# Optimization experiments

Measured on AMD Instinct MI355X. Metric: run time of the kernel, lower is better.

Reference implementation:

```python
import jax, jax.numpy as jnp
import numpy as np

SIGMA = 25.0
N, E, F, D = 10000, 160000, 256, 3


def setup_inputs() -> dict:
    key = jax.random.key(0)
    ks = jax.random.split(key, 24)
    s = 0.02
    inp = {
        "x": jax.random.normal(ks[0], (N, D), jnp.float32),
        "edge_index": jax.random.randint(ks[1], (2, E), 0, N, jnp.int64),
        "t": jax.random.uniform(ks[2], (N, 1), jnp.float32, 1e-3, 1.0),
        "emb_pcs": jax.random.normal(ks[3], (N, F), jnp.float32),
        # x_encoder
        "enc_W": jax.random.normal(ks[4], (D, F), jnp.float32) * s,
        "enc_b": jnp.zeros((F,), jnp.float32),
        # GaussianFourierProjection (scale=30, fixed) + Linear
        "fourier_W": jax.random.normal(ks[5], (F // 2,), jnp.float32) * 30.0,
        "te_W": jax.random.normal(ks[6], (F, F), jnp.float32) * s,
        "te_b": jnp.zeros((F,), jnp.float32),
        # mlp1 / mlp2: Linear(6F,F) -> ReLU -> Linear(F,F)
        "m1_W1": jax.random.normal(ks[7], (6 * F, F), jnp.float32) * s,
        "m1_b1": jnp.zeros((F,), jnp.float32),
        "m1_W2": jax.random.normal(ks[8], (F, F), jnp.float32) * s,
        "m1_b2": jnp.zeros((F,), jnp.float32),
        "m2_W1": jax.random.normal(ks[9], (6 * F, F), jnp.float32) * s,
        "m2_b1": jnp.zeros((F,), jnp.float32),
        "m2_W2": jax.random.normal(ks[10], (F, F), jnp.float32) * s,
        "m2_b2": jnp.zeros((F,), jnp.float32),
        # mlp3: Linear(6F,F) -> ReLU -> Linear(F,D)
        "m3_W1": jax.random.normal(ks[11], (6 * F, F), jnp.float32) * s,
        "m3_b1": jnp.zeros((F,), jnp.float32),
        "m3_W2": jax.random.normal(ks[12], (F, D), jnp.float32) * s,
        "m3_b2": jnp.zeros((D,), jnp.float32),
    }
    return inp


def _edge_conv(h, src, dst, W1, b1, W2, b2, n):
    # PyG EdgeConv: out_i = max_{j->i} MLP([x_i, x_j - x_i])
    hi = h[dst]                                             # [E, 3F]
    e = jnp.concatenate([hi, h[src] - hi], axis=-1)         # [E, 6F]
    e = jax.nn.relu(e @ W1 + b1) @ W2 + b2                  # [E, out]
    out = jax.ops.segment_max(e, dst, num_segments=n)
    return jnp.where(jnp.isfinite(out), out, 0.0)           # empty segments -> 0


def reference(x, edge_index, t, emb_pcs,
              enc_W, enc_b, fourier_W, te_W, te_b,
              m1_W1, m1_b1, m1_W2, m1_b2,
              m2_W1, m2_b1, m2_W2, m2_b2,
              m3_W1, m3_b1, m3_W2, m3_b2):
    src, dst = edge_index[0], edge_index[1]
    n = x.shape[0]
    # time embedding: Fourier projection -> Linear -> swish
    tv = t[:, 0]
    proj = tv[:, None] * fourier_W[None, :] * (2.0 * np.pi)  # [N, F/2]
    temb = jnp.concatenate([jnp.sin(proj), jnp.cos(proj)], axis=-1) @ te_W + te_b
    temb = temb * jax.nn.sigmoid(temb)                       # [N, F]
    h = x @ enc_W + enc_b                                    # [N, F]
    h = jnp.concatenate([h, temb, emb_pcs], axis=-1)         # [N, 3F]
    h = jax.nn.relu(_edge_conv(h, src, dst, m1_W1, m1_b1, m1_W2, m1_b2, n))
    h = jnp.concatenate([h, temb, emb_pcs], axis=-1)
    h = jax.nn.relu(_edge_conv(h, src, dst, m2_W1, m2_b1, m2_W2, m2_b2, n))
    h = jnp.concatenate([h, temb, emb_pcs], axis=-1)
    h = _edge_conv(h, src, dst, m3_W1, m3_b1, m3_W2, m3_b2, n)  # [N, D]
    # marginal_prob_std(t) = sqrt((sigma^(2t) - 1) / (2 ln sigma))
    std = jnp.sqrt((jnp.power(SIGMA, 2.0 * t) - 1.0) / (2.0 * jnp.log(SIGMA)))
    return h / (std + 1e-7)
```

## Files before the change

### kernel.cpp

```cpp
#include <hip/hip_runtime.h>
#include <hip/hip_bf16.h>
#include <math.h>

#define HC 768
#define DPB 8

typedef __attribute__((ext_vector_type(8))) short bf16x8;
typedef __attribute__((ext_vector_type(4))) float f32x4;

__device__ __forceinline__ float bf2f(unsigned short h) {
    return __uint_as_float(((unsigned)h) << 16);
}
__device__ __forceinline__ unsigned short f2bf(float f) {
    unsigned u = __float_as_uint(f);
    return (unsigned short)((u + 0x7fffu + ((u >> 16) & 1u)) >> 16);
}
__device__ __forceinline__ unsigned pack_bf2(float a, float b) {
    __hip_bfloat162 h = __float22bfloat162_rn(make_float2(a, b));
    return *reinterpret_cast<unsigned*>(&h);
}

__device__ __forceinline__ unsigned enc_f(float f) {
    unsigned u = __float_as_uint(f);
    return (u & 0x80000000u) ? ~u : (u | 0x80000000u);
}
__device__ __forceinline__ float dec_f(unsigned e) {
    unsigned u = (e & 0x80000000u) ? (e & 0x7FFFFFFFu) : ~e;
    return __uint_as_float(u);
}
#define ENC_NEG_INF 0x007FFFFFu

__global__ void pre_and_prep_kernel(const float* __restrict__ x,
                                    const float* __restrict__ t,
                                    const float* __restrict__ emb,
                                    const float* __restrict__ enc_W,
                                    const float* __restrict__ enc_b,
                                    const float* __restrict__ fw,
                                    const float* __restrict__ te_W,
                                    const float* __restrict__ te_b,
                                    unsigned short* __restrict__ hcat,
                                    float* __restrict__ invstd,
                                    const float* __restrict__ W1a,
                                    const float* __restrict__ W1b,
                                    const float* __restrict__ W1c,
                                    const float* __restrict__ W2a,
                                    const float* __restrict__ W2b,
                                    const float* __restrict__ W2c,
                                    unsigned short* __restrict__ WcatT,
                                    unsigned short* __restrict__ W2T,
                                    unsigned short* __restrict__ W2T3,
                                    int N, int nPre) {
    __shared__ float smem[64 * 65];
    const int tid = threadIdx.x;

    if ((int)blockIdx.x < nPre) {
        float (*ti)[256] = (float(*)[256])smem;
        float* tv = smem + 8 * 256;
        const int n0 = blockIdx.x * 8;

        if (tid < 8) {
            int n = n0 + tid;
            float tt = (n < N) ? t[n] : 1.0f;
            tv[tid] = tt;
            const float ln_s = 3.2188758248682006f;
            float p = expf(2.0f * tt * ln_s);
            float sd = sqrtf((p - 1.0f) / (2.0f * ln_s));
            if (n < N) invstd[n] = 1.0f / (sd + 1e-7f);
        }
        __syncthreads();

        const float TWO_PI = 6.283185307179586f;
        for (int p = tid; p < 8 * 128; p += 256) {
            int n = p >> 7, j = p & 127;
            float pr = tv[n] * fw[j] * TWO_PI;
            ti[n][j]       = sinf(pr);
            ti[n][j + 128] = cosf(pr);
        }
        __syncthreads();

        const int j = tid;
        float acc[8];
#pragma unroll
        for (int n = 0; n < 8; ++n) acc[n] = 0.f;
        for (int k = 0; k < 256; ++k) {
            float w = te_W[k * 256 + j];
#pragma unroll
            for (int n = 0; n < 8; ++n) acc[n] += ti[n][k] * w;
        }
        float bj  = te_b[j];
        float ew0 = enc_W[0 * 256 + j], ew1 = enc_W[1 * 256 + j], ew2 = enc_W[2 * 256 + j];
        float ebj = enc_b[j];
        for (int n = 0; n < 8; ++n) {
            int node = n0 + n;
            if (node >= N) break;
            float v = acc[n] + bj;
            float temb = v / (1.0f + expf(-v));
            float h0 = x[node * 3 + 0] * ew0 + x[node * 3 + 1] * ew1 +
                       x[node * 3 + 2] * ew2 + ebj;
            hcat[(size_t)node * HC + j]       = f2bf(h0);
            hcat[(size_t)node * HC + 256 + j] = f2bf(temb);
            hcat[(size_t)node * HC + 512 + j] = f2bf(emb[node * 256 + j]);
        }
    } else {
        float (*buf)[65] = (float(*)[65])smem;
        const int bid = blockIdx.x - nPre;
        const int tx = tid & 63, ty = tid >> 6;

        if (bid < 288) {
            const int l = bid / 96, r = bid - l * 96;
            const float* W1 = (l == 0) ? W1a : (l == 1) ? W1b : W1c;
            unsigned short* WT = WcatT + (size_t)l * 512 * 768;
            const int k0 = (r % 12) * 64, n0 = (r / 12) * 64;
#pragma unroll
            for (int i = 0; i < 16; ++i) {
                int kl = ty + i * 4;
                int k = k0 + kl, n = n0 + tx;
                float v = (n < 256) ? (W1[(size_t)k * 256 + n] - W1[(size_t)(k + 768) * 256 + n])
                                    : W1[(size_t)(k + 768) * 256 + (n - 256)];
                buf[kl][tx] = v;
            }
            __syncthreads();
#pragma unroll
            for (int i = 0; i < 16; ++i) {
                int nl = ty + i * 4;
                WT[(size_t)(n0 + nl) * 768 + k0 + tx] = f2bf(buf[tx][nl]);
            }
        } else if (bid < 320) {
            const int m = bid - 288, l = m >> 4, r = m & 15;
            const float* W2 = (l == 0) ? W2a : W2b;
            unsigned short* WT = W2T + (size_t)l * 256 * 256;
            const int k0 = (r & 3) * 64, n0 = (r >> 2) * 64;
#pragma unroll
            for (int i = 0; i < 16; ++i) {
                int kl = ty + i * 4;
                buf[kl][tx] = W2[(size_t)(k0 + kl) * 256 + n0 + tx];
            }
            __syncthreads();
#pragma unroll
            for (int i = 0; i < 16; ++i) {
                int nl = ty + i * 4;
                WT[(size_t)(n0 + nl) * 256 + k0 + tx] = f2bf(buf[tx][nl]);
            }
        } else {
            int idx = (bid - 320) * 256 + tid;
            int n = idx >> 8, k = idx & 255;
            W2T3[idx] = (n < 3) ? f2bf(W2c[(size_t)k * 3 + n]) : (unsigned short)0;
        }
    }
}

__global__ __launch_bounds__(256)
void node_gemm_mfma_kernel(const unsigned short* __restrict__ A,
                           const unsigned short* __restrict__ BT,
                           const float* __restrict__ b1,
                           unsigned short* __restrict__ C,
                           int M) {
    const int row0 = blockIdx.x * 64, col0 = blockIdx.y * 128;
    const int tid = threadIdx.x;
    const int wv = tid >> 6, lane = tid & 63;
    const int q = lane >> 4, nl = lane & 15;
    const int rbase = row0 + (wv >> 1) * 32;
    const int cbase = col0 + (wv & 1) * 64;

    int r0c = min(rbase + nl, M - 1);
    int r1c = min(rbase + 16 + nl, M - 1);
    const unsigned short* pa0 = A + (size_t)r0c * HC + q * 8;
    const unsigned short* pa1 = A + (size_t)r1c * HC + q * 8;

    f32x4 acc[2][4];
#pragma unroll
    for (int s = 0; s < 2; ++s)
#pragma unroll
        for (int t = 0; t < 4; ++t) acc[s][t] = (f32x4){0.f, 0.f, 0.f, 0.f};

    for (int ks = 0; ks < 24; ++ks) {
        const int k0 = ks * 32;
        const bf16x8 av0 = *(const bf16x8*)(pa0 + k0);
        const bf16x8 av1 = *(const bf16x8*)(pa1 + k0);
#pragma unroll
        for (int t = 0; t < 4; ++t) {
            const bf16x8 bv = *(const bf16x8*)(BT + (size_t)(cbase + t * 16 + nl) * 768 + k0 + q * 8);
            acc[0][t] = __builtin_amdgcn_mfma_f32_16x16x32_bf16(av0, bv, acc[0][t], 0, 0, 0);
            acc[1][t] = __builtin_amdgcn_mfma_f32_16x16x32_bf16(av1, bv, acc[1][t], 0, 0, 0);
        }
    }

#pragma unroll
    for (int s = 0; s < 2; ++s) {
        const int rr = rbase + s * 16 + q * 4;
#pragma unroll
        for (int t = 0; t < 4; ++t) {
            int col = cbase + t * 16 + nl;
            float bb = (col < 256) ? b1[col] : 0.f;
#pragma unroll
            for (int i = 0; i < 4; ++i) {
                int r = rr + i;
                if (r < M) C[(size_t)r * 512 + col] = f2bf(acc[s][t][i] + bb);
            }
        }
    }
}

__global__ void init_kernel(unsigned* __restrict__ cnt, unsigned* __restrict__ seg3, int N) {
    int idx = blockIdx.x * 256 + threadIdx.x;
    if (idx < 2 * N) cnt[idx] = 0u;
    else if (idx < 5 * N) seg3[idx - 2 * N] = ENC_NEG_INF;
}
__global__ void hist_kernel(const int* __restrict__ dst, unsigned* __restrict__ cnt, int E) {
    int e = blockIdx.x * 256 + threadIdx.x;
    if (e < E) atomicAdd(&cnt[dst[e]], 1u);
}
__global__ void scan_kernel(const unsigned* __restrict__ cnt,
                            int* __restrict__ row_start, int N) {
    __shared__ unsigned buf[1024];
    __shared__ unsigned carry;
    const int tid = threadIdx.x;
    if (tid == 0) carry = 0u;
    __syncthreads();
    for (int base = 0; base < N; base += 1024) {
        int i = base + tid;
        unsigned v = (i < N) ? cnt[i] : 0u;
        buf[tid] = v;
        __syncthreads();
#pragma unroll
        for (int off = 1; off < 1024; off <<= 1) {
            unsigned add = (tid >= off) ? buf[tid - off] : 0u;
            __syncthreads();
            buf[tid] += add;
            __syncthreads();
        }
        if (i < N) row_start[i] = (int)(carry + buf[tid] - v);
        __syncthreads();
        if (tid == 0) carry += buf[1023];
        __syncthreads();
    }
    if (tid == 0) row_start[N] = (int)carry;
}
__global__ void scatter_kernel(const int* __restrict__ src, const int* __restrict__ dst,
                               const int* __restrict__ row_start,
                               unsigned* __restrict__ wcnt,
                               int* __restrict__ es, int* __restrict__ ed, int E) {
    int e = blockIdx.x * 256 + threadIdx.x;
    if (e >= E) return;
    int d = dst[e];
    int pos = row_start[d] + (int)atomicAdd(&wcnt[d], 1u);
    es[pos] = src[e];
    ed[pos] = d;
}

__global__ __launch_bounds__(256, 3)
void edge_seg_gemm_kernel(const unsigned short* __restrict__ RQb,
                          const int* __restrict__ es,
                          const int* __restrict__ ed,
                          const int* __restrict__ row_start,
                          const unsigned short* __restrict__ W2T,
                          const float* __restrict__ b2,
                          unsigned short* __restrict__ hcat,
                          int N, int E) {
    __shared__ unsigned short af[64][264];
    __shared__ unsigned short rdst[DPB][256];
    __shared__ unsigned lseg[DPB * 256];
    __shared__ int ss[64], sdl[64];
    const int d0 = blockIdx.x * DPB;
    const int tid = threadIdx.x;
    const int wv = tid >> 6, lane = tid & 63;
    const int q = lane >> 4, nl = lane & 15;

    for (int i = tid; i < DPB * 256; i += 256) lseg[i] = ENC_NEG_INF;

    {
        int rrow = tid >> 5;
        int kc = (tid & 31) * 8;
        int d = d0 + rrow;
        int dc = (d < N) ? d : (N - 1);
        *(bf16x8*)&rdst[rrow][kc] = *(const bf16x8*)(RQb + (size_t)dc * 512 + kc);
    }

    const int eBeg = row_start[d0];
    const int eEnd = row_start[min(d0 + DPB, N)];

    for (int c0 = eBeg; c0 < eEnd; c0 += 64) {
        __syncthreads();
        if (tid < 64) {
            int e = c0 + tid;
            ss[tid]  = (e < eEnd) ? es[e] : 0;
            sdl[tid] = (e < eEnd) ? (ed[e] - d0) : -1;
        }
        __syncthreads();

        {
            const int el = tid >> 2;
            const int kc = (tid & 3) * 64;
            int dl = sdl[el];
            int dla = (dl >= 0) ? dl : 0;
            int srow = ss[el];
            const unsigned short* ps = RQb + (size_t)srow * 512 + 256 + kc;
#pragma unroll
            for (int j = 0; j < 8; ++j) {
                bf16x8 dv = *(const bf16x8*)&rdst[dla][kc + j * 8];
                bf16x8 sv = *(const bf16x8*)(ps + j * 8);
                float f[8];
#pragma unroll
                for (int u = 0; u < 8; ++u)
                    f[u] = fmaxf(bf2f((unsigned short)dv[u]) + bf2f((unsigned short)sv[u]), 0.f);
                uint4 o;
                o.x = pack_bf2(f[0], f[1]);
                o.y = pack_bf2(f[2], f[3]);
                o.z = pack_bf2(f[4], f[5]);
                o.w = pack_bf2(f[6], f[7]);
                *(uint4*)&af[el][kc + j * 8] = o;
            }
        }
        __syncthreads();

#pragma unroll
        for (int sub = 0; sub < 4; ++sub) {
            f32x4 acc[4];
#pragma unroll
            for (int t = 0; t < 4; ++t) acc[t] = (f32x4){0.f, 0.f, 0.f, 0.f};
#pragma unroll
            for (int ks = 0; ks < 8; ++ks) {
                const bf16x8 av = *(const bf16x8*)&af[sub * 16 + nl][ks * 32 + q * 8];
#pragma unroll
                for (int t = 0; t < 4; ++t) {
                    const bf16x8 bv = *(const bf16x8*)(W2T +
                        (size_t)(wv * 64 + t * 16 + nl) * 256 + ks * 32 + q * 8);
                    acc[t] = __builtin_amdgcn_mfma_f32_16x16x32_bf16(av, bv, acc[t], 0, 0, 0);
                }
            }
            const int m0 = sub * 16 + q * 4;
            int dls[4];
#pragma unroll
            for (int i = 0; i < 4; ++i) dls[i] = sdl[m0 + i];
#pragma unroll
            for (int t = 0; t < 4; ++t) {
                const int col = wv * 64 + t * 16 + nl;
                float cur = -INFINITY;
                int cd = dls[0];
#pragma unroll
                for (int i = 0; i < 4; ++i) {
                    int dl = dls[i];
                    if (dl != cd) {
                        if (cd >= 0) atomicMax(&lseg[cd * 256 + col], enc_f(cur));
                        cur = -INFINITY; cd = dl;
                    }
                    cur = fmaxf(cur, acc[t][i]);
                }
                if (cd >= 0) atomicMax(&lseg[cd * 256 + col], enc_f(cur));
            }
        }
    }
    __syncthreads();

    for (int i = tid; i < DPB * 256; i += 256) {
        int dl = i >> 8, col = i & 255;
        int d = d0 + dl;
        if (d >= N) continue;
        float f = dec_f(lseg[i]);
        float v = isfinite(f) ? fmaxf(f + b2[col], 0.f) : 0.f;
        hcat[(size_t)d * HC + col] = f2bf(v);
    }
}

__global__ __launch_bounds__(256)
void edge3_mfma_kernel(const unsigned short* __restrict__ RQb,
                       const int* __restrict__ es,
                       const int* __restrict__ ed,
                       const unsigned short* __restrict__ W2T3,
                       const float* __restrict__ b2,
                       unsigned* __restrict__ seg3,
                       int E) {
    const int wave = blockIdx.x * 4 + (threadIdx.x >> 6);
    const int lane = threadIdx.x & 63;
    const int q = lane >> 4, nl = lane & 15;
    const int e0 = wave * 16;
    if (e0 >= E) return;

    bf16x8 bv[8];
#pragma unroll
    for (int ks = 0; ks < 8; ++ks)
        bv[ks] = *(const bf16x8*)(W2T3 + (size_t)nl * 256 + ks * 32 + q * 8);

    int eA = e0 + nl;
    int eAc = (eA < E) ? eA : (E - 1);
    const int dA = ed[eAc], sA = es[eAc];
    const unsigned short* pd = RQb + (size_t)dA * 512 + q * 8;
    const unsigned short* ps = RQb + (size_t)sA * 512 + 256 + q * 8;

    f32x4 acc = (f32x4){0.f, 0.f, 0.f, 0.f};
#pragma unroll
    for (int ks = 0; ks < 8; ++ks) {
        bf16x8 dv = *(const bf16x8*)(pd + ks * 32);
        bf16x8 sv = *(const bf16x8*)(ps + ks * 32);
        float f[8];
#pragma unroll
        for (int u = 0; u < 8; ++u)
            f[u] = fmaxf(bf2f((unsigned short)dv[u]) + bf2f((unsigned short)sv[u]), 0.f);
        uint4 o;
        o.x = pack_bf2(f[0], f[1]);
        o.y = pack_bf2(f[2], f[3]);
        o.z = pack_bf2(f[4], f[5]);
        o.w = pack_bf2(f[6], f[7]);
        bf16x8 av = *(bf16x8*)&o;
        acc = __builtin_amdgcn_mfma_f32_16x16x32_bf16(av, bv[ks], acc, 0, 0, 0);
    }

    if (nl < 3) {
        float bb = b2[nl];
        float cur = -INFINITY;
        int cd = -2;
#pragma unroll
        for (int i = 0; i < 4; ++i) {
            int e = e0 + q * 4 + i;
            int d = (e < E) ? ed[e] : -1;
            if (d != cd) {
                if (cd >= 0) atomicMax(&seg3[(size_t)cd * 3 + nl], enc_f(cur + bb));
                cur = -INFINITY; cd = d;
            }
            if (d >= 0) cur = fmaxf(cur, acc[i]);
        }
        if (cd >= 0) atomicMax(&seg3[(size_t)cd * 3 + nl], enc_f(cur + bb));
    }
}

__global__ void finalize3_kernel(const unsigned* __restrict__ seg3,
                                 const float* __restrict__ invstd,
                                 float* __restrict__ out, int N) {
    int idx = blockIdx.x * 256 + threadIdx.x;
    if (idx >= N * 3) return;
    int n = idx / 3;
    float f = dec_f(seg3[idx]);
    if (!isfinite(f)) f = 0.f;
    out[idx] = f * invstd[n];
}

extern "C" void kernel_launch(void* const* d_in, const int* in_sizes, int n_in,
                              void* d_out, int out_size, void* d_ws, size_t ws_size,
                              hipStream_t stream) {
    const float* x     = (const float*)d_in[0];
    const int*   ei    = (const int*)d_in[1];
    const float* t     = (const float*)d_in[2];
    const float* emb   = (const float*)d_in[3];
    const float* enc_W = (const float*)d_in[4];
    const float* enc_b = (const float*)d_in[5];
    const float* fw    = (const float*)d_in[6];
    const float* te_W  = (const float*)d_in[7];
    const float* te_b  = (const float*)d_in[8];
    const float* W1[3] = {(const float*)d_in[9],  (const float*)d_in[13], (const float*)d_in[17]};
    const float* b1[3] = {(const float*)d_in[10], (const float*)d_in[14], (const float*)d_in[18]};
    const float* W2[3] = {(const float*)d_in[11], (const float*)d_in[15], (const float*)d_in[19]};
    const float* b2[3] = {(const float*)d_in[12], (const float*)d_in[16], (const float*)d_in[20]};

    const int N = in_sizes[2];
    const int E = in_sizes[1] / 2;
    const int* src = ei;
    const int* dst = ei + E;

    char* ws = (char*)d_ws;
    unsigned short* hcat  = (unsigned short*)ws; ws += (size_t)N * HC * 2;
    unsigned short* RQb   = (unsigned short*)ws; ws += (size_t)N * 512 * 2;
    unsigned short* WcatT = (unsigned short*)ws; ws += (size_t)3 * 512 * 768 * 2;
    unsigned short* W2T   = (unsigned short*)ws; ws += (size_t)2 * 256 * 256 * 2;
    unsigned short* W2T3  = (unsigned short*)ws; ws += (size_t)16 * 256 * 2;
    unsigned* seg3        = (unsigned*)ws;       ws += (size_t)N * 3 * 4;
    float*    invstd      = (float*)ws;          ws += (size_t)N * 4;
    int*      es          = (int*)ws;            ws += (size_t)E * 4;
    int*      ed          = (int*)ws;            ws += (size_t)E * 4;
    unsigned* cnt         = (unsigned*)ws;       ws += (size_t)N * 4;
    unsigned* wcnt        = (unsigned*)ws;       ws += (size_t)N * 4;
    int*      row_start   = (int*)ws;            ws += (size_t)(N + 1) * 4;

    init_kernel<<<(5 * N + 255) / 256, 256, 0, stream>>>(cnt, seg3, N);
    hist_kernel<<<(E + 255) / 256, 256, 0, stream>>>(dst, cnt, E);
    scan_kernel<<<1, 1024, 0, stream>>>(cnt, row_start, N);
    scatter_kernel<<<(E + 255) / 256, 256, 0, stream>>>(src, dst, row_start, wcnt, es, ed, E);

    const int nPre = (N + 7) / 8;
    pre_and_prep_kernel<<<nPre + 336, 256, 0, stream>>>(
        x, t, emb, enc_W, enc_b, fw, te_W, te_b, hcat, invstd,
        W1[0], W1[1], W1[2], W2[0], W2[1], W2[2], WcatT, W2T, W2T3, N, nPre);

    for (int l = 0; l < 3; ++l) {
        dim3 gn((N + 63) / 64, 4);
        node_gemm_mfma_kernel<<<gn, 256, 0, stream>>>(
            hcat, WcatT + (size_t)l * 512 * 768, b1[l], RQb, N);
        if (l < 2) {
            edge_seg_gemm_kernel<<<(N + DPB - 1) / DPB, 256, 0, stream>>>(
                RQb, es, ed, row_start, W2T + (size_t)l * 256 * 256, b2[l], hcat, N, E);
        } else {
            int chunks = (E + 15) / 16;
            edge3_mfma_kernel<<<(chunks + 3) / 4, 256, 0, stream>>>(
                RQb, es, ed, W2T3, b2[l], seg3, E);
            finalize3_kernel<<<(N * 3 + 255) / 256, 256, 0, stream>>>(seg3, invstd, (float*)d_out, N);
        }
    }
}
```

Measured before the change: 503.0 us.

## Double-buffer edge tiles with register prefetch and use wave-shuffle scan

Restructures the edge segment GEMM to process edges in 32-row chunks with a double-buffered LDS A tile. The source-row gathers for the next chunk are prefetched into registers while the current chunk's MFMAs run, and one sync per chunk is removed. The shared src/dst index staging is dropped: destination indices are read directly from global memory in the epilogue. Separately, the scan kernel's log-step shared-memory scan with many barriers is replaced by a wave-level shuffle scan plus a small cross-wave scan.

```diff
diff --git a/kernel.cpp b/kernel.cpp
--- a/kernel.cpp
+++ b/kernel.cpp
@@ -212,26 +212,38 @@
 }
 __global__ void scan_kernel(const unsigned* __restrict__ cnt,
                             int* __restrict__ row_start, int N) {
-    __shared__ unsigned buf[1024];
+    __shared__ unsigned wexc[16];
+    __shared__ unsigned chunk_total;
     __shared__ unsigned carry;
-    const int tid = threadIdx.x;
+    const int tid = threadIdx.x, wv = tid >> 6, ln = tid & 63;
     if (tid == 0) carry = 0u;
     __syncthreads();
     for (int base = 0; base < N; base += 1024) {
         int i = base + tid;
         unsigned v = (i < N) ? cnt[i] : 0u;
-        buf[tid] = v;
-        __syncthreads();
-#pragma unroll
-        for (int off = 1; off < 1024; off <<= 1) {
-            unsigned add = (tid >= off) ? buf[tid - off] : 0u;
-            __syncthreads();
-            buf[tid] += add;
-            __syncthreads();
-        }
-        if (i < N) row_start[i] = (int)(carry + buf[tid] - v);
-        __syncthreads();
-        if (tid == 0) carry += buf[1023];
+        unsigned s = v;
+#pragma unroll
+        for (int off = 1; off < 64; off <<= 1) {
+            unsigned o = __shfl_up(s, off);
+            if (ln >= off) s += o;
+        }
+        if (ln == 63) wexc[wv] = s;
+        __syncthreads();
+        if (tid < 16) {
+            unsigned ws = wexc[tid];
+            unsigned tt = ws;
+#pragma unroll
+            for (int off = 1; off < 16; off <<= 1) {
+                unsigned o = __shfl_up(tt, off);
+                if (tid >= off) tt += o;
+            }
+            wexc[tid] = tt - ws;
+            if (tid == 15) chunk_total = tt;
+        }
+        __syncthreads();
+        if (i < N) row_start[i] = (int)(carry + wexc[wv] + s - v);
+        __syncthreads();
+        if (tid == 0) carry += chunk_total;
         __syncthreads();
     }
     if (tid == 0) row_start[N] = (int)carry;
@@ -257,10 +269,9 @@
                           const float* __restrict__ b2,
                           unsigned short* __restrict__ hcat,
                           int N, int E) {
-    __shared__ unsigned short af[64][264];
+    __shared__ unsigned short af[2][32][264];
     __shared__ unsigned short rdst[DPB][256];
     __shared__ unsigned lseg[DPB * 256];
-    __shared__ int ss[64], sdl[64];
     const int d0 = blockIdx.x * DPB;
     const int tid = threadIdx.x;
     const int wv = tid >> 6, lane = tid & 63;
@@ -278,27 +289,36 @@
 
     const int eBeg = row_start[d0];
     const int eEnd = row_start[min(d0 + DPB, N)];
-
-    for (int c0 = eBeg; c0 < eEnd; c0 += 64) {
-        __syncthreads();
-        if (tid < 64) {
-            int e = c0 + tid;
-            ss[tid]  = (e < eEnd) ? es[e] : 0;
-            sdl[tid] = (e < eEnd) ? (ed[e] - d0) : -1;
-        }
-        __syncthreads();
+    const int H = (eEnd - eBeg + 31) >> 5;
+
+    const int el = tid >> 3;
+    const int kb = (tid & 7) * 8;
+
+    __syncthreads();
+
+    uint4 svr[4];
+    int sdl_c = -1;
+    {
+        int e = eBeg + el;
+        int ec = min(e, eEnd - 1); if (ec < 0) ec = 0;
+        int srow = es[ec];
+        sdl_c = (e < eEnd) ? (ed[ec] - d0) : -1;
+        const unsigned short* ps = RQb + (size_t)srow * 512 + 256;
+#pragma unroll
+        for (int j = 0; j < 4; ++j) svr[j] = *(const uint4*)(ps + kb + j * 64);
+    }
+
+    for (int h = 0; h < H; ++h) {
+        const int b = h & 1;
+        const int c0 = eBeg + h * 32;
 
         {
-            const int el = tid >> 2;
-            const int kc = (tid & 3) * 64;
-            int dl = sdl[el];
-            int dla = (dl >= 0) ? dl : 0;
-            int srow = ss[el];
-            const unsigned short* ps = RQb + (size_t)srow * 512 + 256 + kc;
-#pragma unroll
-            for (int j = 0; j < 8; ++j) {
-                bf16x8 dv = *(const bf16x8*)&rdst[dla][kc + j * 8];
-                bf16x8 sv = *(const bf16x8*)(ps + j * 8);
+            int dla = (sdl_c >= 0) ? sdl_c : 0;
+#pragma unroll
+            for (int j = 0; j < 4; ++j) {
+                const int k = kb + j * 64;
+                bf16x8 dv = *(const bf16x8*)&rdst[dla][k];
+                bf16x8 sv = *(bf16x8*)&svr[j];
                 float f[8];
 #pragma unroll
                 for (int u = 0; u < 8; ++u)
@@ -308,30 +328,48 @@
                 o.y = pack_bf2(f[2], f[3]);
                 o.z = pack_bf2(f[4], f[5]);
                 o.w = pack_bf2(f[6], f[7]);
-                *(uint4*)&af[el][kc + j * 8] = o;
-            }
-        }
-        __syncthreads();
-
-#pragma unroll
-        for (int sub = 0; sub < 4; ++sub) {
-            f32x4 acc[4];
-#pragma unroll
-            for (int t = 0; t < 4; ++t) acc[t] = (f32x4){0.f, 0.f, 0.f, 0.f};
-#pragma unroll
-            for (int ks = 0; ks < 8; ++ks) {
-                const bf16x8 av = *(const bf16x8*)&af[sub * 16 + nl][ks * 32 + q * 8];
-#pragma unroll
-                for (int t = 0; t < 4; ++t) {
-                    const bf16x8 bv = *(const bf16x8*)(W2T +
-                        (size_t)(wv * 64 + t * 16 + nl) * 256 + ks * 32 + q * 8);
-                    acc[t] = __builtin_amdgcn_mfma_f32_16x16x32_bf16(av, bv, acc[t], 0, 0, 0);
-                }
-            }
+                *(uint4*)&af[b][el][k] = o;
+            }
+        }
+        __syncthreads();
+
+        if (h + 1 < H) {
+            int e = c0 + 32 + el;
+            int ec = min(e, eEnd - 1);
+            int srow = es[ec];
+            sdl_c = (e < eEnd) ? (ed[ec] - d0) : -1;
+            const unsigned short* ps = RQb + (size_t)srow * 512 + 256;
+#pragma unroll
+            for (int j = 0; j < 4; ++j) svr[j] = *(const uint4*)(ps + kb + j * 64);
+        }
+
+        f32x4 acc[2][4];
+#pragma unroll
+        for (int s = 0; s < 2; ++s)
+#pragma unroll
+            for (int t = 0; t < 4; ++t) acc[s][t] = (f32x4){0.f, 0.f, 0.f, 0.f};
+#pragma unroll
+        for (int ks = 0; ks < 8; ++ks) {
+            const bf16x8 a0 = *(const bf16x8*)&af[b][nl][ks * 32 + q * 8];
+            const bf16x8 a1 = *(const bf16x8*)&af[b][16 + nl][ks * 32 + q * 8];
+#pragma unroll
+            for (int t = 0; t < 4; ++t) {
+                const bf16x8 bv = *(const bf16x8*)(W2T +
+                    (size_t)(wv * 64 + t * 16 + nl) * 256 + ks * 32 + q * 8);
+                acc[0][t] = __builtin_amdgcn_mfma_f32_16x16x32_bf16(a0, bv, acc[0][t], 0, 0, 0);
+                acc[1][t] = __builtin_amdgcn_mfma_f32_16x16x32_bf16(a1, bv, acc[1][t], 0, 0, 0);
+            }
+        }
+
+#pragma unroll
+        for (int sub = 0; sub < 2; ++sub) {
             const int m0 = sub * 16 + q * 4;
             int dls[4];
 #pragma unroll
-            for (int i = 0; i < 4; ++i) dls[i] = sdl[m0 + i];
+            for (int i = 0; i < 4; ++i) {
+                int e = c0 + m0 + i;
+                dls[i] = (e < eEnd) ? (ed[e] - d0) : -1;
+            }
 #pragma unroll
             for (int t = 0; t < 4; ++t) {
                 const int col = wv * 64 + t * 16 + nl;
@@ -344,7 +382,7 @@
                         if (cd >= 0) atomicMax(&lseg[cd * 256 + col], enc_f(cur));
                         cur = -INFINITY; cd = dl;
                     }
-                    cur = fmaxf(cur, acc[t][i]);
+                    cur = fmaxf(cur, acc[sub][t][i]);
                 }
                 if (cd >= 0) atomicMax(&lseg[cd * 256 + col], enc_f(cur));
             }
```

Result: slower. 586.2 us (+16.5%).
